# Performance work log

Measured on AMD Instinct MI355X. Metric: run time of the kernel, lower is better.

## Reference

```python
import jax, jax.numpy as jnp
import numpy as np

N, C, H, T, D, K = 4096, 512, 128, 64, 20, 10


def setup_inputs() -> dict:
    key = jax.random.key(0)
    ks = jax.random.split(key, 40)
    s = 0.05
    inp = {}
    inp["x"] = jax.random.normal(ks[0], (N, D * T), jnp.float32)
    inp["concept_matrix"] = (jax.random.uniform(ks[1], (N, C)) < 0.05).astype(jnp.float32)
    inp["market_value"] = jax.random.uniform(ks[2], (N,), jnp.float32) + 0.1
    # GRU params (torch layout: w_ih [3H,in], w_hh [3H,H], biases [3H]); 2 layers
    inp["gru_w_ih0"] = jax.random.normal(ks[3], (3 * H, D), jnp.float32) * s
    inp["gru_w_hh0"] = jax.random.normal(ks[4], (3 * H, H), jnp.float32) * s
    inp["gru_b_ih0"] = jax.random.normal(ks[5], (3 * H,), jnp.float32) * s
    inp["gru_b_hh0"] = jax.random.normal(ks[6], (3 * H,), jnp.float32) * s
    inp["gru_w_ih1"] = jax.random.normal(ks[7], (3 * H, H), jnp.float32) * s
    inp["gru_w_hh1"] = jax.random.normal(ks[8], (3 * H, H), jnp.float32) * s
    inp["gru_b_ih1"] = jax.random.normal(ks[9], (3 * H,), jnp.float32) * s
    inp["gru_b_hh1"] = jax.random.normal(ks[10], (3 * H,), jnp.float32) * s
    names = ["ps", "hs", "ps_fore", "hs_fore", "ps_back", "hs_back", "indi"]
    for i, n in enumerate(names):
        inp["w_" + n] = jax.random.normal(ks[11 + 2 * i], (H, H), jnp.float32) * s
        inp["b_" + n] = jax.random.normal(ks[12 + 2 * i], (H,), jnp.float32) * s
    inp["w_out"] = jax.random.normal(ks[30], (1, H), jnp.float32) * s
    inp["b_out"] = jax.random.normal(ks[31], (1,), jnp.float32) * s
    return inp


def _cos_sim(x, y):
    # x [n,d], y [m,d] -> [n,m]; NaN (0/0) replaced by 0 via safe denominator
    xy = x @ y.T
    nx = jnp.sqrt(jnp.sum(x * x, axis=1))[:, None]
    ny = jnp.sqrt(jnp.sum(y * y, axis=1))[:, None]
    return xy / jnp.maximum(nx @ ny.T, 1e-12)


def _gru_layer(seq, wih, whh, bih, bhh):
    # seq [T, n, in] -> outputs [T, n, H]
    n = seq.shape[1]
    h0 = jnp.zeros((n, whh.shape[1]), seq.dtype)

    def step(h, xt):
        gx = xt @ wih.T + bih
        gh = h @ whh.T + bhh
        gxr, gxz, gxn = jnp.split(gx, 3, axis=1)
        ghr, ghz, ghn = jnp.split(gh, 3, axis=1)
        r = jax.nn.sigmoid(gxr + ghr)
        z = jax.nn.sigmoid(gxz + ghz)
        ncand = jnp.tanh(gxn + r * ghn)
        hnew = (1.0 - z) * ncand + z * h
        return hnew, hnew

    _, out = jax.lax.scan(step, h0, seq)
    return out


def reference(x, concept_matrix, market_value,
              gru_w_ih0, gru_w_hh0, gru_b_ih0, gru_b_hh0,
              gru_w_ih1, gru_w_hh1, gru_b_ih1, gru_b_hh1,
              w_ps, b_ps, w_hs, b_hs, w_ps_fore, b_ps_fore, w_hs_fore, b_hs_fore,
              w_ps_back, b_ps_back, w_hs_back, b_hs_back, w_indi, b_indi,
              w_out, b_out):
    n = x.shape[0]
    # [n, D*T] -> [n, D, T] -> [n, T, D] -> [T, n, D]
    seq = jnp.swapaxes(x.reshape(n, D, -1).transpose(0, 2, 1), 0, 1)
    out0 = _gru_layer(seq, gru_w_ih0, gru_w_hh0, gru_b_ih0, gru_b_hh0)
    out1 = _gru_layer(out0, gru_w_ih1, gru_w_hh1, gru_b_ih1, gru_b_hh1)
    x_hidden = out1[-1]  # [n, H]

    # --- predefined-concept branch ---
    s2c = concept_matrix * market_value[:, None]
    s2c_den = jnp.sum(s2c, axis=0)[None, :] * concept_matrix + 1.0
    s2c = s2c / s2c_den
    hidden = s2c.T @ x_hidden  # [C, H]
    v1 = jnp.sum(hidden, axis=1) != 0  # valid concepts (replaces row filtering)
    s2c2 = jax.nn.softmax(x_hidden @ hidden.T, axis=0)  # [n, C], column-wise
    hidden2 = s2c2.T @ x_hidden  # [C, H]
    c2s = _cos_sim(x_hidden, hidden2)
    c2s = jax.nn.softmax(jnp.where(v1[None, :], c2s, -1e9), axis=1) * v1[None, :]
    p_shared = c2s @ hidden2
    p_shared = p_shared @ w_ps.T + b_ps
    p_back = p_shared @ w_ps_back.T + b_ps_back
    out_ps = jax.nn.leaky_relu(p_shared @ w_ps_fore.T + b_ps_fore)

    # --- hidden-concept branch ---
    h_shared = x_hidden - p_back
    hs2c = _cos_sim(h_shared, h_shared)  # [n, n]
    diag = jnp.diagonal(hs2c)
    hs2c = hs2c * (1.0 - jnp.eye(n, dtype=hs2c.dtype))
    _, idx = jax.lax.top_k(hs2c, K)  # [n, K]
    mask = jnp.zeros_like(hs2c).at[jnp.arange(n)[:, None], idx].set(1.0)
    hs2c = hs2c * mask
    hs2c = hs2c + jnp.diag((jnp.sum(hs2c, axis=0) != 0).astype(hs2c.dtype) * diag)
    hidden_h = (h_shared.T @ hs2c).T  # [n, H]
    v2 = jnp.sum(hidden_h, axis=1) != 0
    hc2s = _cos_sim(h_shared, hidden_h)
    hc2s = jax.nn.softmax(jnp.where(v2[None, :], hc2s, -1e9), axis=1) * v2[None, :]
    h_si = hc2s @ hidden_h
    h_si = h_si @ w_hs.T + b_hs
    h_back = h_si @ w_hs_back.T + b_hs_back
    out_hs = jax.nn.leaky_relu(h_si @ w_hs_fore.T + b_hs_fore)

    # --- individual branch + head ---
    indi = x_hidden - p_back - h_back
    out_indi = jax.nn.leaky_relu(indi @ w_indi.T + b_indi)
    all_info = out_ps + out_hs + out_indi
    return (all_info @ w_out.T + b_out).squeeze()
```

## Files before the change

### kernel.cpp

```cpp
#include <hip/hip_runtime.h>
#include <cstddef>

#define NR 4096
#define CDIM 512
#define HDIM 128
#define TSTEPS 64
#define DDIM 20
#define KTOP 10

typedef __attribute__((ext_vector_type(8))) short short8;
typedef __attribute__((ext_vector_type(4))) float f32x4;

__device__ __forceinline__ unsigned short f2bf(float f) {
    union { float f; unsigned u; } x; x.f = f;
    unsigned r = (x.u + 0x7fffu + ((x.u >> 16) & 1u)) >> 16;
    return (unsigned short)r;
}
__device__ __forceinline__ unsigned short f2bf_t(float f) {
    union { float f; unsigned u; } x; x.f = f;
    return (unsigned short)(x.u >> 16);
}
__device__ __forceinline__ float bf2f(unsigned short h) {
    union { unsigned u; float f; } x; x.u = ((unsigned)h) << 16;
    return x.f;
}
__device__ __forceinline__ float sigm(float v) {
    return __builtin_amdgcn_rcpf(1.f + __expf(-v));
}
__device__ __forceinline__ float tanh_f(float v) {
    return 1.f - 2.f * __builtin_amdgcn_rcpf(1.f + __expf(2.f * v));
}

#define MFMA16(a, b, c) __builtin_amdgcn_mfma_f32_16x16x32_bf16(a, b, c, 0, 0, 0)

struct MG {
    const float* A; const unsigned short* Bh; const unsigned short* Bl;
    const float* bias; float* C; const float* aux; float* sub;
    const unsigned short* Ah; const unsigned short* Al;
    const unsigned short* Bh2; const unsigned short* Bl2;
    const float* bias2; float* C2;
    const float* wout; const float* bout; float* hout;
    int N, K, kchunk, flags, flags2;
};

__global__ __launch_bounds__(256) void mfma_gemm(MG g)
{
    const int tid = threadIdx.x;
    const int w = tid >> 6, lane = tid & 63, quad = lane >> 4, lm = lane & 15;
    const int bm = (blockIdx.y << 6) + (w << 4);
    const int bn = blockIdx.x << 6;
    const int NC = g.K >> 5;
    int flags = g.flags;
    const unsigned short* Bh = g.Bh;
    const unsigned short* Bl = g.Bl;
    const float* bias = g.bias;
    float* C = g.C;
    int zk = blockIdx.z;
    if (g.flags & 32) {
        if (blockIdx.z) { Bh = g.Bh2; Bl = g.Bl2; bias = g.bias2; C = g.C2; flags = g.flags2; }
        zk = 0;
    }
    const int c0 = (zk * g.kchunk) >> 5;
    const int c1 = c0 + (g.kchunk >> 5);
    const float* arow = g.A + (size_t)(bm + lm) * g.K;
    const int packA = g.flags & 16;
    f32x4 acc[4];
    #pragma unroll
    for (int t = 0; t < 4; t++) acc[t] = (f32x4){0.f, 0.f, 0.f, 0.f};

    for (int c = c0; c < c1; c++) {
        short8 ah, al;
        if (packA) {
            size_t aidx = ((size_t)((bm >> 4) * NC + c) * 64 + lane) * 8;
            ah = *(const short8*)(g.Ah + aidx);
            al = *(const short8*)(g.Al + aidx);
        } else {
            const float* ap = arow + (c << 5) + (quad << 3);
            float4 a0 = *(const float4*)ap;
            float4 a1 = *(const float4*)(ap + 4);
            #pragma unroll
            for (int jj = 0; jj < 4; jj++) {
                float f = (&a0.x)[jj];
                unsigned short h = f2bf(f);
                ah[jj] = h; al[jj] = f2bf_t(f - bf2f(h));
                f = (&a1.x)[jj];
                h = f2bf(f);
                ah[4 + jj] = h; al[4 + jj] = f2bf_t(f - bf2f(h));
            }
        }
        #pragma unroll
        for (int t = 0; t < 4; t++) {
            size_t bidx = ((size_t)(((bn >> 4) + t) * NC + c) * 64 + lane) * 8;
            short8 bh = *(const short8*)(Bh + bidx);
            short8 bl = *(const short8*)(Bl + bidx);
            acc[t] = MFMA16(ah, bh, acc[t]);
            acc[t] = MFMA16(ah, bl, acc[t]);
            acc[t] = MFMA16(al, bh, acc[t]);
        }
    }
    float rsum[4] = {0.f, 0.f, 0.f, 0.f};
    #pragma unroll
    for (int t = 0; t < 4; t++) {
        #pragma unroll
        for (int rg = 0; rg < 4; rg++) {
            int row = bm + (quad << 2) + rg;
            int col = bn + (t << 4) + lm;
            float v = acc[t][rg];
            if (flags & 1) v += bias[col];
            if (flags & 2) v = v > 0.f ? v : 0.01f * v;
            if (flags & 64) rsum[rg] += v * g.wout[col];
            if (!(flags & 128)) {
                if (flags & 4) atomicAdd(&C[(size_t)row * g.N + col], v);
                else C[(size_t)row * g.N + col] = v;
            }
            if (flags & 8)
                g.sub[(size_t)row * g.N + col] = g.aux[(size_t)row * g.N + col] - v;
        }
    }
    if (flags & 64) {
        #pragma unroll
        for (int rg = 0; rg < 4; rg++) {
            #pragma unroll
            for (int d = 1; d < 16; d <<= 1) rsum[rg] += __shfl_xor(rsum[rg], d);
        }
        if (lm == 0) {
            #pragma unroll
            for (int rg = 0; rg < 4; rg++) {
                float s = rsum[rg];
                if ((flags & 256) && bn == 0) s += g.bout[0];
                atomicAdd(&g.hout[bm + (quad << 2) + rg], s);
            }
        }
    }
}

__global__ void pack_bt(const float* __restrict__ src, unsigned short* __restrict__ hi,
                        unsigned short* __restrict__ lo, int K, int total)
{
    int idx = blockIdx.x * 256 + threadIdx.x;
    if (idx >= total) return;
    int NC = K >> 5;
    int lane = idx & 63;
    int c = (idx >> 6) % NC;
    int t = idx / (NC * 64);
    int n = (t << 4) + (lane & 15);
    int kb = (c << 5) + ((lane >> 4) << 3);
    #pragma unroll
    for (int j = 0; j < 8; j++) {
        float f = src[(size_t)n * K + kb + j];
        unsigned short h = f2bf(f);
        hi[(size_t)idx * 8 + j] = h;
        lo[(size_t)idx * 8 + j] = f2bf_t(f - bf2f(h));
    }
}

__global__ void pack_both(const float* __restrict__ src,
                          unsigned short* __restrict__ bth, unsigned short* __restrict__ btl,
                          unsigned short* __restrict__ knh, unsigned short* __restrict__ knl,
                          int N, int total_kn)
{
    int idx = blockIdx.x * 256 + threadIdx.x;
    int lane = idx & 63;
    int totBT = (N >> 4) * 256;
    if (idx < totBT) {
        int c = (idx >> 6) & 3;
        int t = idx >> 8;
        int n = (t << 4) + (lane & 15);
        int kb = (c << 5) + ((lane >> 4) << 3);
        #pragma unroll
        for (int j = 0; j < 8; j++) {
            float f = src[(size_t)n * HDIM + kb + j];
            unsigned short h = f2bf(f);
            bth[(size_t)idx * 8 + j] = h;
            btl[(size_t)idx * 8 + j] = f2bf_t(f - bf2f(h));
        }
    }
    if (idx < total_kn) {
        int NC = N >> 5;
        int c = (idx >> 6) % NC;
        int t = idx / (NC * 64);
        int n = (t << 4) + (lane & 15);
        int kb = (c << 5) + ((lane >> 4) << 3);
        #pragma unroll
        for (int j = 0; j < 8; j++) {
            float f = src[(size_t)(kb + j) * HDIM + n];
            unsigned short h = f2bf(f);
            knh[(size_t)idx * 8 + j] = h;
            knl[(size_t)idx * 8 + j] = f2bf_t(f - bf2f(h));
        }
    }
}

struct W7 {
    const float* src[7];
    unsigned short* hi[7];
    unsigned short* lo[7];
};
__global__ void pack_w7(W7 p)
{
    int idx = blockIdx.x * 256 + threadIdx.x;
    if (idx >= 7 * 2048) return;
    int m = idx >> 11;
    int r = idx & 2047;
    int lane = r & 63;
    int c = (r >> 6) & 3;
    int t = r >> 8;
    int n = (t << 4) + (lane & 15);
    int kb = (c << 5) + ((lane >> 4) << 3);
    const float* src = p.src[m];
    unsigned short* hi = p.hi[m];
    unsigned short* lo = p.lo[m];
    #pragma unroll
    for (int j = 0; j < 8; j++) {
        float f = src[(size_t)n * HDIM + kb + j];
        unsigned short h = f2bf(f);
        hi[(size_t)r * 8 + j] = h;
        lo[(size_t)r * 8 + j] = f2bf_t(f - bf2f(h));
    }
}

__global__ __launch_bounds__(256) void scan_topk(const float* __restrict__ S,
        const float* __restrict__ hn, float* __restrict__ diagv,
        float* __restrict__ tvals, int* __restrict__ tidx)
{
    int row = blockIdx.x;
    const float* d = S + (size_t)row * NR;
    int tid = threadIdx.x;
    int wv = tid >> 6, lane = tid & 63;
    float hi_ = hn[row];
    float lv[16];
    #pragma unroll
    for (int i = 0; i < 16; i++) {
        int j = tid + (i << 8);
        float v = d[j] / fmaxf(hi_ * hn[j], 1e-12f);
        if (j == row) { diagv[row] = v; v = 0.f; }
        lv[i] = v;
    }
    __shared__ float sv[4];
    __shared__ int si[4];
    for (int k = 0; k < KTOP; k++) {
        float bv = -INFINITY; int bi = 0x7fffffff;
        #pragma unroll
        for (int i = 0; i < 16; i++) {
            int j = tid + (i << 8);
            if (lv[i] > bv || (lv[i] == bv && j < bi)) { bv = lv[i]; bi = j; }
        }
        #pragma unroll
        for (int m = 1; m < 64; m <<= 1) {
            float ov = __shfl_xor(bv, m); int oi = __shfl_xor(bi, m);
            if (ov > bv || (ov == bv && oi < bi)) { bv = ov; bi = oi; }
        }
        if (lane == 0) { sv[wv] = bv; si[wv] = bi; }
        __syncthreads();
        bv = sv[0]; bi = si[0];
        #pragma unroll
        for (int w = 1; w < 4; w++) {
            float ov = sv[w]; int oi = si[w];
            if (ov > bv || (ov == bv && oi < bi)) { bv = ov; bi = oi; }
        }
        if (tid == 0) { tvals[row * KTOP + k] = bv; tidx[row * KTOP + k] = bi; }
        if ((bi & 255) == tid) lv[bi >> 8] = -INFINITY;
        __syncthreads();
    }
}

__global__ __launch_bounds__(512) void hc2s_flash(
    const float* __restrict__ hsh, const float* __restrict__ hn,
    const float* __restrict__ hhn, const float* __restrict__ v2,
    const unsigned short* __restrict__ Bh, const unsigned short* __restrict__ Bl,
    const unsigned short* __restrict__ Vh, const unsigned short* __restrict__ Vl,
    float* __restrict__ pO, float* __restrict__ pM, float* __restrict__ pL)
{
    __shared__ __attribute__((aligned(16))) unsigned short Ph[8][16 * 72];
    __shared__ __attribute__((aligned(16))) unsigned short Plo[8][16 * 72];

    const int tid = threadIdx.x;
    const int wv = tid >> 6, lane = tid & 63, quad = lane >> 4, lm = lane & 15;
    const int rg2 = wv >> 1;
    const int cc = wv & 1;
    const int bm = (blockIdx.x << 6) + (rg2 << 4);
    const int rgg = (blockIdx.x << 2) + rg2;
    const int pidx = (blockIdx.y << 1) + cc;
    const int jt0 = (blockIdx.y << 4) + (cc << 3);

    short8 ahh[4], ahl[4];
    #pragma unroll
    for (int c = 0; c < 4; c++) {
        const float* ap = hsh + (size_t)(bm + lm) * HDIM + (c << 5) + (quad << 3);
        float4 a0 = *(const float4*)ap;
        float4 a1 = *(const float4*)(ap + 4);
        #pragma unroll
        for (int j = 0; j < 4; j++) {
            float f = (&a0.x)[j];
            unsigned short h = f2bf(f);
            ahh[c][j] = h; ahl[c][j] = f2bf_t(f - bf2f(h));
            f = (&a1.x)[j];
            h = f2bf(f);
            ahh[c][4 + j] = h; ahl[c][4 + j] = f2bf_t(f - bf2f(h));
        }
    }
    float hnr[4];
    #pragma unroll
    for (int rg = 0; rg < 4; rg++) hnr[rg] = hn[bm + (quad << 2) + rg];

    float m_old[4], l_old[4];
    #pragma unroll
    for (int rg = 0; rg < 4; rg++) { m_old[rg] = -INFINITY; l_old[rg] = 0.f; }
    f32x4 o[8];
    #pragma unroll
    for (int vt = 0; vt < 8; vt++) o[vt] = (f32x4){0.f, 0.f, 0.f, 0.f};

    const int pwr = lm * 72;
    for (int it = 0; it < 8; it++) {
        const int jt = jt0 + it;
        f32x4 s[4];
        #pragma unroll
        for (int tg = 0; tg < 4; tg++) {
            s[tg] = (f32x4){0.f, 0.f, 0.f, 0.f};
            #pragma unroll
            for (int c = 0; c < 4; c++) {
                size_t bidx = ((size_t)(((jt << 2) + tg) * 4 + c) * 64 + lane) * 8;
                short8 bh = *(const short8*)(Bh + bidx);
                short8 bl = *(const short8*)(Bl + bidx);
                s[tg] = MFMA16(ahh[c], bh, s[tg]);
                s[tg] = MFMA16(ahh[c], bl, s[tg]);
                s[tg] = MFMA16(ahl[c], bh, s[tg]);
            }
        }
        float sv[4][4];
        #pragma unroll
        for (int tg = 0; tg < 4; tg++) {
            int col = (jt << 6) + (tg << 4) + lm;
            float hc = hhn[col];
            float vm = v2[col];
            #pragma unroll
            for (int rg = 0; rg < 4; rg++) {
                float v = s[tg][rg] * __builtin_amdgcn_rcpf(fmaxf(hnr[rg] * hc, 1e-12f));
                sv[tg][rg] = (vm == 0.f) ? -1e9f : v;
            }
        }
        float m_new[4], alpha[4], tsum[4], pv[4][4];
        #pragma unroll
        for (int rg = 0; rg < 4; rg++) {
            float m = fmaxf(fmaxf(sv[0][rg], sv[1][rg]), fmaxf(sv[2][rg], sv[3][rg]));
            #pragma unroll
            for (int d = 1; d < 16; d <<= 1) m = fmaxf(m, __shfl_xor(m, d));
            m_new[rg] = fmaxf(m_old[rg], m);
            alpha[rg] = __expf(m_old[rg] - m_new[rg]);
        }
        #pragma unroll
        for (int rg = 0; rg < 4; rg++) {
            float p0_ = __expf(sv[0][rg] - m_new[rg]);
            float p1_ = __expf(sv[1][rg] - m_new[rg]);
            float p2_ = __expf(sv[2][rg] - m_new[rg]);
            float p3_ = __expf(sv[3][rg] - m_new[rg]);
            pv[0][rg] = p0_; pv[1][rg] = p1_; pv[2][rg] = p2_; pv[3][rg] = p3_;
            float ss = p0_ + p1_ + p2_ + p3_;
            #pragma unroll
            for (int d = 1; d < 16; d <<= 1) ss += __shfl_xor(ss, d);
            tsum[rg] = ss;
        }
        #pragma unroll
        for (int rg = 0; rg < 4; rg++) {
            l_old[rg] = l_old[rg] * alpha[rg] + tsum[rg];
            m_old[rg] = m_new[rg];
        }
        #pragma unroll
        for (int vt = 0; vt < 8; vt++) {
            #pragma unroll
            for (int rg = 0; rg < 4; rg++) o[vt][rg] *= alpha[rg];
        }
        #pragma unroll
        for (int tg = 0; tg < 4; tg++) {
            #pragma unroll
            for (int rg = 0; rg < 4; rg++) {
                int off = ((quad << 2) + rg) * 72 + (tg << 4) + lm;
                float p = pv[tg][rg];
                unsigned short h = f2bf(p);
                Ph[wv][off] = h;
                Plo[wv][off] = f2bf_t(p - bf2f(h));
            }
        }
        __asm__ volatile("s_waitcnt lgkmcnt(0)" ::: "memory");
        #pragma unroll
        for (int c2 = 0; c2 < 2; c2++) {
            int poff = pwr + (c2 << 5) + (quad << 3);
            short8 pah = *(const short8*)&Ph[wv][poff];
            short8 pal = *(const short8*)&Plo[wv][poff];
            int cg = (jt << 1) + c2;
            #pragma unroll
            for (int vt = 0; vt < 8; vt++) {
                size_t b0 = ((size_t)(vt * 128 + cg) * 64 + lane) * 8;
                short8 vh = *(const short8*)(Vh + b0);
                short8 vl = *(const short8*)(Vl + b0);
                o[vt] = MFMA16(pah, vh, o[vt]);
                o[vt] = MFMA16(pah, vl, o[vt]);
                o[vt] = MFMA16(pal, vh, o[vt]);
            }
        }
    }
    size_t pb = ((size_t)rgg * 8 + pidx) * 16;
    #pragma unroll
    for (int rg = 0; rg < 4; rg++) {
        int r = (quad << 2) + rg;
        #pragma unroll
        for (int vt = 0; vt < 8; vt++)
            pO[(pb + r) * 128 + (vt << 4) + lm] = o[vt][rg];
    }
    if (lm == 0) {
        #pragma unroll
        for (int rg = 0; rg < 4; rg++) {
            int r = (quad << 2) + rg;
            pM[pb + r] = m_old[rg];
            pL[pb + r] = l_old[rg];
        }
    }
}

__global__ __launch_bounds__(256) void hc2s_merge(const float* __restrict__ pO,
        const float* __restrict__ pM, const float* __restrict__ pL,
        float* __restrict__ O)
{
    int rgg = blockIdx.x;
    int tid = threadIdx.x;
    int r = tid >> 4;
    int c0 = (tid & 15) << 3;
    float m[8], e[8];
    float M = -INFINITY;
    #pragma unroll
    for (int i = 0; i < 8; i++) {
        m[i] = pM[((size_t)rgg * 8 + i) * 16 + r];
        M = fmaxf(M, m[i]);
    }
    float L = 0.f;
    #pragma unroll
    for (int i = 0; i < 8; i++) {
        e[i] = __expf(m[i] - M);
        L += pL[((size_t)rgg * 8 + i) * 16 + r] * e[i];
    }
    float invL = __builtin_amdgcn_rcpf(L);
    float a[8];
    #pragma unroll
    for (int k = 0; k < 8; k++) a[k] = 0.f;
    #pragma unroll
    for (int i = 0; i < 8; i++) {
        const float* src = pO + (((size_t)rgg * 8 + i) * 16 + r) * 128 + c0;
        float4 v0 = *(const float4*)src;
        float4 v1 = *(const float4*)(src + 4);
        a[0] += v0.x * e[i]; a[1] += v0.y * e[i]; a[2] += v0.z * e[i]; a[3] += v0.w * e[i];
        a[4] += v1.x * e[i]; a[5] += v1.y * e[i]; a[6] += v1.z * e[i]; a[7] += v1.w * e[i];
    }
    float* dst = O + ((size_t)rgg * 16 + r) * 128 + c0;
    #pragma unroll
    for (int k = 0; k < 8; k++) dst[k] = a[k] * invL;
}

__global__ void pack_wb(const float* __restrict__ W, unsigned short* __restrict__ Wp,
                        int K, int nch)
{
    int idx = blockIdx.x * 256 + threadIdx.x;
    if (idx >= 24 * nch * 64) return;
    int lane = idx & 63;
    int c = (idx >> 6) % nch;
    int t = idx / (nch * 64);
    int n = t * 16 + (lane & 15);
    int kb = c * 32 + (lane >> 4) * 8;
    #pragma unroll
    for (int j = 0; j < 8; j++) {
        int k = kb + j;
        float f = (k < K) ? W[(size_t)n * K + k] : 0.f;
        Wp[(size_t)idx * 8 + j] = f2bf(f);
    }
}

__global__ __launch_bounds__(512, 2) void gru_mfma(
    const float* __restrict__ xg,
    const unsigned short* __restrict__ wih0p,
    const unsigned short* __restrict__ whh0p,
    const unsigned short* __restrict__ wih1p,
    const unsigned short* __restrict__ whh1p,
    const float* __restrict__ bih0, const float* __restrict__ bhh0,
    const float* __restrict__ bih1, const float* __restrict__ bhh1,
    float* __restrict__ xh)
{
    __shared__ __attribute__((aligned(16))) unsigned short h0A[2][2][16 * 136];
    __shared__ __attribute__((aligned(16))) unsigned short h1A[2][2][16 * 136];
    __shared__ __attribute__((aligned(16))) unsigned short xA[2][2][16 * 40];

    const int tid = threadIdx.x;
    const int w2 = tid >> 6;
    const int lane = tid & 63;
    const int quad = lane >> 4;
    const int lm = lane & 15;
    const int n0 = blockIdx.x << 4;
    const int j = (w2 << 4) + lm;

    for (int i = tid; i < 2 * 2 * 16 * 136; i += 512) {
        ((unsigned short*)h0A)[i] = 0;
        ((unsigned short*)h1A)[i] = 0;
    }
    for (int i = tid; i < 2 * 2 * 16 * 40; i += 512) ((unsigned short*)xA)[i] = 0;

    float br0 = bih0[j] + bhh0[j];
    float bz0 = bih0[128 + j] + bhh0[128 + j];
    float bni0 = bih0[256 + j];
    float bnh0 = bhh0[256 + j];
    float br1 = bih1[j] + bhh1[j];
    float bz1 = bih1[128 + j] + bhh1[128 + j];
    float bni1 = bih1[256 + j];
    float bnh1 = bhh1[256 + j];

    short8 W0x[3], W0h[3][4], W1x[3][4], W1h[3][4];
    {
        const int lb = lane * 8;
        W0x[0] = *(const short8*)&wih0p[(size_t)(w2) * 512 + lb];
        W0x[1] = *(const short8*)&wih0p[(size_t)(8 + w2) * 512 + lb];
        W0x[2] = *(const short8*)&wih0p[(size_t)(16 + w2) * 512 + lb];
        #pragma unroll
        for (int c = 0; c < 4; c++) {
            W0h[0][c] = *(const short8*)&whh0p[(size_t)((w2) * 4 + c) * 512 + lb];
            W0h[1][c] = *(const short8*)&whh0p[(size_t)((8 + w2) * 4 + c) * 512 + lb];
            W0h[2][c] = *(const short8*)&whh0p[(size_t)((16 + w2) * 4 + c) * 512 + lb];
            W1x[0][c] = *(const short8*)&wih1p[(size_t)((w2) * 4 + c) * 512 + lb];
            W1x[1][c] = *(const short8*)&wih1p[(size_t)((8 + w2) * 4 + c) * 512 + lb];
            W1x[2][c] = *(const short8*)&wih1p[(size_t)((16 + w2) * 4 + c) * 512 + lb];
            W1h[0][c] = *(const short8*)&whh1p[(size_t)((w2) * 4 + c) * 512 + lb];
            W1h[1][c] = *(const short8*)&whh1p[(size_t)((8 + w2) * 4 + c) * 512 + lb];
            W1h[2][c] = *(const short8*)&whh1p[(size_t)((16 + w2) * 4 + c) * 512 + lb];
        }
    }

    const int aoff = lm * 136 + quad * 8;
    const int xoff = lm * 40 + quad * 8;
    const bool stager = tid < 16 * DDIM;
    const int sn = tid / DDIM, sd = tid % DDIM;
    const float* xrow = xg + (size_t)(n0 + sn) * (DDIM * TSTEPS) + sd * TSTEPS;
    const int soff = sn * 40 + sd;

    float h0reg[4] = {0.f, 0.f, 0.f, 0.f};
    float h1reg[4] = {0.f, 0.f, 0.f, 0.f};

    if (stager) {
        float v0 = xrow[0], v1 = xrow[1];
        unsigned short a = f2bf_t(v0);
        xA[0][0][soff] = a; xA[0][1][soff] = f2bf_t(v0 - bf2f(a));
        unsigned short b = f2bf_t(v1);
        xA[1][0][soff] = b; xA[1][1][soff] = f2bf_t(v1 - bf2f(b));
    }
    __syncthreads();

    {
        f32x4 accr = (f32x4){br0, br0, br0, br0};
        f32x4 accz = (f32x4){bz0, bz0, bz0, bz0};
        f32x4 accni = (f32x4){bni0, bni0, bni0, bni0};
        short8 axh = *(const short8*)&xA[0][0][xoff];
        short8 axl = *(const short8*)&xA[0][1][xoff];
        accr = MFMA16(axh, W0x[0], accr);
        accr = MFMA16(axl, W0x[0], accr);
        accz = MFMA16(axh, W0x[1], accz);
        accz = MFMA16(axl, W0x[1], accz);
        accni = MFMA16(axh, W0x[2], accni);
        accni = MFMA16(axl, W0x[2], accni);
        #pragma unroll
        for (int rg = 0; rg < 4; rg++) {
            float r = sigm(accr[rg]);
            float z = sigm(accz[rg]);
            float nc = tanh_f(accni[rg] + r * bnh0);
            float hnew = nc - z * nc;
            h0reg[rg] = hnew;
            int off = (quad * 4 + rg) * 136 + j;
            unsigned short hh_ = f2bf_t(hnew);
            h0A[0][0][off] = hh_;
            h0A[0][1][off] = f2bf_t(hnew - bf2f(hh_));
        }
    }
    __syncthreads();

#define GRU_IT(B, DO_L0, XT, LAST)                                                \
{                                                                                 \
    float xv = 0.f;                                                               \
    if ((XT) >= 0 && stager) xv = xrow[XT];          \
    f32x4 accr0 = (f32x4){br0, br0, br0, br0};                                    \
    f32x4 accz0 = (f32x4){bz0, bz0, bz0, bz0};                                    \
    f32x4 accni0 = (f32x4){bni0, bni0, bni0, bni0};                               \
    f32x4 accnh0 = (f32x4){bnh0, bnh0, bnh0, bnh0};                               \
    f32x4 accr1 = (f32x4){br1, br1, br1, br1};                                    \
    f32x4 accz1 = (f32x4){bz1, bz1, bz1, bz1};                                    \
    f32x4 accni1 = (f32x4){bni1, bni1, bni1, bni1};                               \
    f32x4 accnh1 = (f32x4){bnh1, bnh1, bnh1, bnh1};                               \
    if (DO_L0) {                                                                  \
        short8 axh = *(const short8*)&xA[(B) ^ 1][0][xoff];                       \
        short8 axl = *(const short8*)&xA[(B) ^ 1][1][xoff];                       \
        accr0 = MFMA16(axh, W0x[0], accr0);                                       \
        accr0 = MFMA16(axl, W0x[0], accr0);                                       \
        accz0 = MFMA16(axh, W0x[1], accz0);                                       \
        accz0 = MFMA16(axl, W0x[1], accz0);                                       \
        accni0 = MFMA16(axh, W0x[2], accni0);                                     \
        accni0 = MFMA16(axl, W0x[2], accni0);                                     \
    }                                                                             \
    _Pragma("unroll")                                                             \
    for (int c = 0; c < 4; c++) {                                                 \
        short8 a0h = *(const short8*)&h0A[B][0][aoff + c * 32];                   \
        short8 a0l = *(const short8*)&h0A[B][1][aoff + c * 32];                   \
        if (DO_L0) {                                                              \
            accr0 = MFMA16(a0h, W0h[0][c], accr0);                                \
            accr0 = MFMA16(a0l, W0h[0][c], accr0);                                \
            accz0 = MFMA16(a0h, W0h[1][c], accz0);                                \
            accz0 = MFMA16(a0l, W0h[1][c], accz0);                                \
            accnh0 = MFMA16(a0h, W0h[2][c], accnh0);                              \
            accnh0 = MFMA16(a0l, W0h[2][c], accnh0);                              \
        }                                                                         \
        accr1 = MFMA16(a0h, W1x[0][c], accr1);                                    \
        accr1 = MFMA16(a0l, W1x[0][c], accr1);                                    \
        accz1 = MFMA16(a0h, W1x[1][c], accz1);                                    \
        accz1 = MFMA16(a0l, W1x[1][c], accz1);                                    \
        accni1 = MFMA16(a0h, W1x[2][c], accni1);                                  \
        accni1 = MFMA16(a0l, W1x[2][c], accni1);                                  \
        short8 a1h = *(const short8*)&h1A[(B) ^ 1][0][aoff + c * 32];             \
        short8 a1l = *(const short8*)&h1A[(B) ^ 1][1][aoff + c * 32];             \
        accr1 = MFMA16(a1h, W1h[0][c], accr1);                                    \
        accr1 = MFMA16(a1l, W1h[0][c], accr1);                                    \
        accz1 = MFMA16(a1h, W1h[1][c], accz1);                                    \
        accz1 = MFMA16(a1l, W1h[1][c], accz1);                                    \
        accnh1 = MFMA16(a1h, W1h[2][c], accnh1);                                  \
        accnh1 = MFMA16(a1l, W1h[2][c], accnh1);                                  \
    }                                                                             \
    if (DO_L0) {                                                                  \
        _Pragma("unroll")                                                         \
        for (int rg = 0; rg < 4; rg++) {                                          \
            float r = sigm(accr0[rg]);                                            \
            float z = sigm(accz0[rg]);                                            \
            float nc = tanh_f(accni0[rg] + r * accnh0[rg]);                       \
            float hnew = nc + z * (h0reg[rg] - nc);                               \
            h0reg[rg] = hnew;                                                     \
            int off = (quad * 4 + rg) * 136 + j;                                  \
            unsigned short hh_ = f2bf_t(hnew);                                    \
            h0A[(B) ^ 1][0][off] = hh_;                                           \
            h0A[(B) ^ 1][1][off] = f2bf_t(hnew - bf2f(hh_));                      \
        }                                                                         \
    }                                                                             \
    _Pragma("unroll")                                                             \
    for (int rg = 0; rg < 4; rg++) {                                              \
        float r = sigm(accr1[rg]);                                                \
        float z = sigm(accz1[rg]);                                                \
        float nc = tanh_f(accni1[rg] + r * accnh1[rg]);                           \
        float hnew = nc + z * (h1reg[rg] - nc);                                   \
        h1reg[rg] = hnew;                                                         \
        if (LAST) {                                                               \
            xh[(size_t)(n0 + quad * 4 + rg) * HDIM + j] = hnew;                   \
        } else {                                                                  \
            int off = (quad * 4 + rg) * 136 + j;                                  \
            unsigned short hh_ = f2bf_t(hnew);                                    \
            h1A[B][0][off] = hh_;                                                 \
            h1A[B][1][off] = f2bf_t(hnew - bf2f(hh_));                            \
        }                                                                         \
    }                                                                             \
    if ((XT) >= 0 && stager) {                                                    \
        unsigned short hh_ = f2bf_t(xv);                                          \
        xA[B][0][soff] = hh_;                                                     \
        xA[B][1][soff] = f2bf_t(xv - bf2f(hh_));                                  \
    }                                                                             \
    if (!(LAST)) __syncthreads();                                                 \
}

    for (int i = 0; i < 62; i += 2) {
        GRU_IT(0, true, i + 2, false)
        GRU_IT(1, true, i + 3, false)
    }
    GRU_IT(0, true, -1, false)
    GRU_IT(1, false, -1, true)
#undef GRU_IT
}

__global__ __launch_bounds__(256) void den_atomic(const float* __restrict__ cm,
        const float* __restrict__ mv, float* __restrict__ den)
{
    int c = blockIdx.x * 64 + (threadIdx.x & 63);
    int rg = threadIdx.x >> 6;
    int nbase = blockIdx.y * 128;
    float acc = 0.f;
    for (int i = 0; i < 32; i++) {
        int n = nbase + rg + (i << 2);
        acc += cm[(size_t)n * CDIM + c] * mv[n];
    }
    __shared__ float red[4][64];
    red[rg][threadIdx.x & 63] = acc;
    __syncthreads();
    if (rg == 0)
        atomicAdd(&den[c], red[0][threadIdx.x] + red[1][threadIdx.x] +
                           red[2][threadIdx.x] + red[3][threadIdx.x]);
}

__global__ __launch_bounds__(256) void s2ct_trans(const float* __restrict__ cm,
        const float* __restrict__ mv, const float* __restrict__ den,
        float* __restrict__ s2cT)
{
    __shared__ float tile[64][65];
    __shared__ float mvs[64];
    const int tid = threadIdx.x;
    const int n0 = blockIdx.x << 6;
    const int c0 = blockIdx.y << 6;
    const int lc = tid & 63, lr = tid >> 6;
    if (tid < 64) mvs[tid] = mv[n0 + tid];
    #pragma unroll
    for (int i = 0; i < 16; i++) {
        int n = lr + (i << 2);
        tile[n][lc] = cm[(size_t)(n0 + n) * CDIM + c0 + lc];
    }
    __syncthreads();
    #pragma unroll
    for (int i = 0; i < 16; i++) {
        int c = lr + (i << 2);
        float m = tile[lc][c];
        float d = den[c0 + c];
        s2cT[(size_t)(c0 + c) * NR + n0 + lc] = (m * mvs[lc]) / (d * m + 1.f);
    }
}

__global__ void row_norm(const float* __restrict__ a, float* __restrict__ out)
{
    int r = blockIdx.x;
    float acc = 0.f;
    for (int h = threadIdx.x; h < HDIM; h += 64) {
        float v = a[(size_t)r * HDIM + h];
        acc += v * v;
    }
    for (int o = 32; o > 0; o >>= 1) acc += __shfl_down(acc, o);
    if (threadIdx.x == 0) out[r] = sqrtf(acc);
}

__global__ void row_nonzero(const float* __restrict__ a, float* __restrict__ out)
{
    int r = blockIdx.x;
    float acc = 0.f;
    for (int h = threadIdx.x; h < HDIM; h += 64) acc += a[(size_t)r * HDIM + h];
    for (int o = 32; o > 0; o >>= 1) acc += __shfl_down(acc, o);
    if (threadIdx.x == 0) out[r] = (acc != 0.f) ? 1.f : 0.f;
}

__global__ void row_norm_nz(const float* __restrict__ a, float* __restrict__ nrm,
                            float* __restrict__ nz)
{
    int r = blockIdx.x;
    float acc = 0.f, s = 0.f;
    for (int h = threadIdx.x; h < HDIM; h += 64) {
        float v = a[(size_t)r * HDIM + h];
        acc += v * v;
        s += v;
    }
    for (int o = 32; o > 0; o >>= 1) { acc += __shfl_down(acc, o); s += __shfl_down(s, o); }
    if (threadIdx.x == 0) { nrm[r] = sqrtf(acc); nz[r] = (s != 0.f) ? 1.f : 0.f; }
}

__global__ __launch_bounds__(256) void cos_softmax_row(float* __restrict__ data, int N,
        const float* __restrict__ rn, const float* __restrict__ cn,
        const float* __restrict__ vmask)
{
    int row = blockIdx.x;
    float* d = data + (size_t)row * N;
    int tid = threadIdx.x;
    int wv = tid >> 6, lane = tid & 63;
    __shared__ float red[8];
    float rnv = rn ? rn[row] : 0.f;
    float mx = -INFINITY;
    for (int j = tid; j < N; j += 256) {
        float v = d[j];
        if (cn) v = v * __builtin_amdgcn_rcpf(fmaxf(rnv * cn[j], 1e-12f));
        if (vmask && vmask[j] == 0.f) v = -1e9f;
        d[j] = v;
        mx = fmaxf(mx, v);
    }
    #pragma unroll
    for (int m = 1; m < 64; m <<= 1) mx = fmaxf(mx, __shfl_xor(mx, m));
    if (lane == 0) red[wv] = mx;
    __syncthreads();
    float M = fmaxf(fmaxf(red[0], red[1]), fmaxf(red[2], red[3]));
    float sum = 0.f;
    for (int j = tid; j < N; j += 256) {
        float e = __expf(d[j] - M);
        d[j] = e;
        sum += e;
    }
    #pragma unroll
    for (int m = 1; m < 64; m <<= 1) sum += __shfl_xor(sum, m);
    if (lane == 0) red[4 + wv] = sum;
    __syncthreads();
    float inv = __builtin_amdgcn_rcpf(red[4] + red[5] + red[6] + red[7]);
    for (int j = tid; j < N; j += 256) {
        float v = d[j] * inv;
        if (vmask) v *= vmask[j];
        d[j] = v;
    }
}

__global__ void hh_scatter(const float* __restrict__ vals, const int* __restrict__ idxs,
                           const float* __restrict__ hsh, float* __restrict__ hh,
                           float* __restrict__ colsum)
{
    int i = blockIdx.x;
    int t = threadIdx.x;
    float hv = hsh[(size_t)i * HDIM + t];
    #pragma unroll
    for (int k = 0; k < KTOP; k++) {
        int p = i * KTOP + k;
        int jj = idxs[p];
        float v = vals[p];
        atomicAdd(&hh[(size_t)jj * HDIM + t], v * hv);
    }
    if (t < KTOP) {
        int p = i * KTOP + t;
        atomicAdd(&colsum[idxs[p]], vals[p]);
    }
}

__global__ void hh_diag(const float* __restrict__ colsum, const float* __restrict__ diag,
                        const float* __restrict__ hsh, float* __restrict__ hh)
{
    int idx = blockIdx.x * 256 + threadIdx.x;
    int j = idx >> 7;
    if (colsum[j] != 0.f) hh[idx] += diag[j] * hsh[idx];
}

static inline void mg(hipStream_t s, const float* A, const unsigned short* Bh,
                      const unsigned short* Bl, const float* bias, float* C,
                      int M, int N, int K, int z, int flags,
                      const float* aux = nullptr, float* sub = nullptr,
                      const unsigned short* Ah = nullptr, const unsigned short* Al = nullptr,
                      const float* wout = nullptr, const float* bout = nullptr,
                      float* hout = nullptr)
{
    MG g{A, Bh, Bl, bias, C, aux, sub, Ah, Al,
         nullptr, nullptr, nullptr, nullptr, wout, bout, hout,
         N, K, K / z, flags | (z > 1 ? 4 : 0) | (Ah ? 16 : 0), 0};
    mfma_gemm<<<dim3(N / 64, M / 64, z), 256, 0, s>>>(g);
}
static inline void mg_dual(hipStream_t s, const float* A,
                           const unsigned short* Bh, const unsigned short* Bl,
                           const float* bias, float* C, int flags1,
                           const unsigned short* Bh2, const unsigned short* Bl2,
                           const float* bias2, float* C2, int flags2,
                           int M, int N, int K,
                           const float* aux, float* sub,
                           const float* wout, const float* bout, float* hout)
{
    MG g{A, Bh, Bl, bias, C, aux, sub, nullptr, nullptr,
         Bh2, Bl2, bias2, C2, wout, bout, hout,
         N, K, K, flags1 | 32, flags2};
    mfma_gemm<<<dim3(N / 64, M / 64, 2), 256, 0, s>>>(g);
}
static inline void pbt(hipStream_t s, const float* src, unsigned short* hi,
                       unsigned short* lo, int N, int K)
{
    int total = (N / 16) * (K / 32) * 64;
    pack_bt<<<(total + 255) / 256, 256, 0, s>>>(src, hi, lo, K, total);
}
static inline void pboth(hipStream_t s, const float* src,
                         unsigned short* bth, unsigned short* btl,
                         unsigned short* knh, unsigned short* knl, int N)
{
    int totBT = (N / 16) * 4 * 64;
    int totKN = 8 * (N / 32) * 64;
    int tot = totBT > totKN ? totBT : totKN;
    pack_both<<<(tot + 255) / 256, 256, 0, s>>>(src, bth, btl, knh, knl, N, totKN);
}

extern "C" void kernel_launch(void* const* d_in, const int* in_sizes, int n_in,
                              void* d_out, int out_size, void* d_ws, size_t ws_size,
                              hipStream_t stream)
{
    (void)in_sizes; (void)n_in; (void)out_size; (void)ws_size;
    const float* x    = (const float*)d_in[0];
    const float* cm   = (const float*)d_in[1];
    const float* mv   = (const float*)d_in[2];
    const float* wih0 = (const float*)d_in[3];
    const float* whh0 = (const float*)d_in[4];
    const float* bih0 = (const float*)d_in[5];
    const float* bhh0 = (const float*)d_in[6];
    const float* wih1 = (const float*)d_in[7];
    const float* whh1 = (const float*)d_in[8];
    const float* bih1 = (const float*)d_in[9];
    const float* bhh1 = (const float*)d_in[10];
    const float* w_ps = (const float*)d_in[11];
    const float* b_ps = (const float*)d_in[12];
    const float* w_hs = (const float*)d_in[13];
    const float* b_hs = (const float*)d_in[14];
    const float* w_ps_fore = (const float*)d_in[15];
    const float* b_ps_fore = (const float*)d_in[16];
    const float* w_hs_fore = (const float*)d_in[17];
    const float* b_hs_fore = (const float*)d_in[18];
    const float* w_ps_back = (const float*)d_in[19];
    const float* b_ps_back = (const float*)d_in[20];
    const float* w_hs_back = (const float*)d_in[21];
    const float* b_hs_back = (const float*)d_in[22];
    const float* w_indi = (const float*)d_in[23];
    const float* b_indi = (const float*)d_in[24];
    const float* w_out  = (const float*)d_in[25];
    const float* b_out  = (const float*)d_in[26];
    float* out = (float*)d_out;

    float* ws = (float*)d_ws;
    float* BIG = ws;
    float* zero0 = ws + 16777216;
    float* den      = zero0;
    float* hidden   = den + 512;
    float* hidden2  = hidden + 65536;
    float* colsum   = hidden2 + 65536;
    float* p0       = colsum + 4096;
    float* hidden_h = p0 + 524288;
    const size_t ZERO_FLOATS = 512 + 65536 + 65536 + 4096 + 524288 + 524288;
    float* h1 = hidden_h + 524288;
    float* v1 = h1 + 524288;
    float* xnorm = v1 + 512;
    float* h2n = xnorm + 4096;
    float* p_shared = h2n + 512;
    float* p_back = p_shared + 524288;
    float* h_shared = p_back + 524288;
    float* hn = h_shared + 524288;
    float* diagv = hn + 4096;
    float* tvals = diagv + 4096;
    int*   tidx = (int*)(tvals + 40960);
    float* v2 = (float*)(tidx + 40960);
    float* hhn = v2 + 4096;
    float* hsi0 = hhn + 4096;
    float* h_si = hsi0 + 524288;
    float* h_back = h_si + 524288;
    float* indi = h_back + 524288;
    float* extra = indi + 524288;

    unsigned short* wih0p = (unsigned short*)(BIG + 5242880);
    unsigned short* whh0p = wih0p + 12288;
    unsigned short* wih1p = whh0p + 49152;
    unsigned short* whh1p = wih1p + 49152;
    float* s2cT = BIG;
    float* L    = BIG + 2097152;
    float* c2s  = BIG + 4194304;
    unsigned short* PB = (unsigned short*)(BIG + 6291456);
    unsigned short* pbt_xh_hi = PB;
    unsigned short* pbt_xh_lo = pbt_xh_hi + 524288;
    unsigned short* pkn_xh_hi = pbt_xh_lo + 524288;
    unsigned short* pkn_xh_lo = pkn_xh_hi + 524288;
    unsigned short* pbt_h2_hi = pkn_xh_lo + 524288;
    unsigned short* pbt_h2_lo = pbt_h2_hi + 65536;
    unsigned short* pkn_h2_hi = pbt_h2_lo + 65536;
    unsigned short* pkn_h2_lo = pkn_h2_hi + 65536;
    unsigned short* wps_hi  = pkn_h2_lo + 65536;
    unsigned short* wps_lo  = wps_hi + 16384;
    unsigned short* wpsb_hi = wps_lo + 16384;
    unsigned short* wpsb_lo = wpsb_hi + 16384;
    unsigned short* wpsf_hi = wpsb_lo + 16384;
    unsigned short* wpsf_lo = wpsf_hi + 16384;
    unsigned short* pbt_hsh_hi = (unsigned short*)p0;
    unsigned short* pbt_hsh_lo = pbt_hsh_hi + 524288;
    unsigned short* pbt_hh_hi = (unsigned short*)indi;
    unsigned short* pbt_hh_lo = pbt_hh_hi + 524288;
    unsigned short* pkn_hh_hi = (unsigned short*)hsi0;
    unsigned short* pkn_hh_lo = pkn_hh_hi + 524288;
    float* part_O = BIG;
    float* part_m = BIG + 4194304;
    float* part_l = BIG + 4227072;
    unsigned short* EX = (unsigned short*)extra;
    unsigned short* whs_hi  = EX;            unsigned short* whs_lo  = EX + 16384;
    unsigned short* whsb_hi = EX + 32768;    unsigned short* whsb_lo = EX + 49152;
    unsigned short* whsf_hi = EX + 65536;    unsigned short* whsf_lo = EX + 81920;
    unsigned short* wind_hi = EX + 98304;    unsigned short* wind_lo = EX + 114688;

    hipMemsetAsync(zero0, 0, ZERO_FLOATS * sizeof(float), stream);
    hipMemsetAsync(out, 0, NR * sizeof(float), stream);

    pack_wb<<<6, 256, 0, stream>>>(wih0, wih0p, DDIM, 1);
    pack_wb<<<24, 256, 0, stream>>>(whh0, whh0p, HDIM, 4);
    pack_wb<<<24, 256, 0, stream>>>(wih1, wih1p, HDIM, 4);
    pack_wb<<<24, 256, 0, stream>>>(whh1, whh1p, HDIM, 4);
    {
        W7 w7;
        w7.src[0] = w_ps;      w7.hi[0] = wps_hi;  w7.lo[0] = wps_lo;
        w7.src[1] = w_ps_back; w7.hi[1] = wpsb_hi; w7.lo[1] = wpsb_lo;
        w7.src[2] = w_ps_fore; w7.hi[2] = wpsf_hi; w7.lo[2] = wpsf_lo;
        w7.src[3] = w_hs;      w7.hi[3] = whs_hi;  w7.lo[3] = whs_lo;
        w7.src[4] = w_hs_back; w7.hi[4] = whsb_hi; w7.lo[4] = whsb_lo;
        w7.src[5] = w_hs_fore; w7.hi[5] = whsf_hi; w7.lo[5] = whsf_lo;
        w7.src[6] = w_indi;    w7.hi[6] = wind_hi; w7.lo[6] = wind_lo;
        pack_w7<<<56, 256, 0, stream>>>(w7);
    }
    gru_mfma<<<NR / 16, 512, 0, stream>>>(x, wih0p, whh0p, wih1p, whh1p,
                                          bih0, bhh0, bih1, bhh1, h1);
    float* x_hidden = h1;

    den_atomic<<<dim3(CDIM / 64, 32), 256, 0, stream>>>(cm, mv, den);
    s2ct_trans<<<dim3(NR / 64, CDIM / 64), 256, 0, stream>>>(cm, mv, den, s2cT);
    pboth(stream, x_hidden, pbt_xh_hi, pbt_xh_lo, pkn_xh_hi, pkn_xh_lo, NR);
    mg(stream, s2cT, pkn_xh_hi, pkn_xh_lo, nullptr, hidden, CDIM, HDIM, NR, 16, 0);
    row_nonzero<<<CDIM, 64, 0, stream>>>(hidden, v1);
    mg(stream, hidden, pbt_xh_hi, pbt_xh_lo, nullptr, L, CDIM, NR, HDIM, 1, 0);
    cos_softmax_row<<<CDIM, 256, 0, stream>>>(L, NR, nullptr, nullptr, nullptr);
    mg(stream, L, pkn_xh_hi, pkn_xh_lo, nullptr, hidden2, CDIM, HDIM, NR, 16, 0);
    row_norm<<<NR, 64, 0, stream>>>(x_hidden, xnorm);
    row_norm<<<CDIM, 64, 0, stream>>>(hidden2, h2n);
    pboth(stream, hidden2, pbt_h2_hi, pbt_h2_lo, pkn_h2_hi, pkn_h2_lo, CDIM);
    mg(stream, x_hidden, pbt_h2_hi, pbt_h2_lo, nullptr, c2s, NR, CDIM, HDIM, 1, 0,
       nullptr, nullptr, pbt_xh_hi, pbt_xh_lo);
    cos_softmax_row<<<NR, 256, 0, stream>>>(c2s, CDIM, xnorm, h2n, v1);
    mg(stream, c2s, pkn_h2_hi, pkn_h2_lo, nullptr, p0, NR, HDIM, CDIM, 4, 0);
    mg(stream, p0, wps_hi, wps_lo, b_ps, p_shared, NR, HDIM, HDIM, 1, 1);
    mg_dual(stream, p_shared,
            wpsb_hi, wpsb_lo, b_ps_back, p_back, 1 | 8,
            wpsf_hi, wpsf_lo, b_ps_fore, nullptr, 1 | 2 | 64 | 128,
            NR, HDIM, HDIM, x_hidden, h_shared, w_out, b_out, out);

    row_norm<<<NR, 64, 0, stream>>>(h_shared, hn);
    pbt(stream, h_shared, pbt_hsh_hi, pbt_hsh_lo, NR, HDIM);
    mg(stream, h_shared, pbt_hsh_hi, pbt_hsh_lo, nullptr, BIG, NR, NR, HDIM, 1, 0,
       nullptr, nullptr, pbt_hsh_hi, pbt_hsh_lo);
    scan_topk<<<NR, 256, 0, stream>>>(BIG, hn, diagv, tvals, tidx);
    hh_scatter<<<NR, HDIM, 0, stream>>>(tvals, tidx, h_shared, hidden_h, colsum);
    hh_diag<<<2048, 256, 0, stream>>>(colsum, diagv, h_shared, hidden_h);
    row_norm_nz<<<NR, 64, 0, stream>>>(hidden_h, hhn, v2);
    pboth(stream, hidden_h, pbt_hh_hi, pbt_hh_lo, pkn_hh_hi, pkn_hh_lo, NR);
    hc2s_flash<<<dim3(NR / 64, 4), 512, 0, stream>>>(h_shared, hn, hhn, v2,
                                                     pbt_hh_hi, pbt_hh_lo,
                                                     pkn_hh_hi, pkn_hh_lo,
                                                     part_O, part_m, part_l);
    hc2s_merge<<<NR / 16, 256, 0, stream>>>(part_O, part_m, part_l, hsi0);
    mg(stream, hsi0, whs_hi, whs_lo, b_hs, h_si, NR, HDIM, HDIM, 1, 1);
    mg_dual(stream, h_si,
            whsb_hi, whsb_lo, b_hs_back, h_back, 1 | 8,
            whsf_hi, whsf_lo, b_hs_fore, nullptr, 1 | 2 | 64 | 128,
            NR, HDIM, HDIM, h_shared, indi, w_out, b_out, out);

    mg(stream, indi, wind_hi, wind_lo, b_indi, nullptr, NR, HDIM, HDIM, 1,
       1 | 2 | 64 | 128 | 256, nullptr, nullptr, nullptr, nullptr,
       w_out, b_out, out);
}
```

Baseline: 697.1 us.

## Merge weight-pack kernels, reorder GRU MFMAs, split-K small bias GEMMs

The four pack_wb launches and pack_w7 become a single pack_all kernel, which cuts launch overhead. In the GRU, MFMA issue order is interleaved so that independent accumulators sit between dependent ones, and the h1 LDS loads are hoisted earlier to hide MFMA dependency latency. The two 128x128 projection GEMMs now use split-K of 2 with atomic accumulation. To support that, bias is added only by the first K-split and p_shared/h_si move into the zeroed region. The atomics add contention and make the summation order nondeterministic.

```diff
diff --git a/kernel.cpp b/kernel.cpp
--- a/kernel.cpp
+++ b/kernel.cpp
@@ -106,7 +106,7 @@
             int row = bm + (quad << 2) + rg;
             int col = bn + (t << 4) + lm;
             float v = acc[t][rg];
-            if (flags & 1) v += bias[col];
+            if ((flags & 1) && (!(flags & 4) || zk == 0)) v += bias[col];
             if (flags & 2) v = v > 0.f ? v : 0.01f * v;
             if (flags & 64) rsum[rg] += v * g.wout[col];
             if (!(flags & 128)) {
@@ -191,31 +191,60 @@
     }
 }
 
-struct W7 {
-    const float* src[7];
-    unsigned short* hi[7];
-    unsigned short* lo[7];
+struct PAll {
+    const float* wb_src[4];
+    unsigned short* wb_dst[4];
+    const float* w7_src[7];
+    unsigned short* w7_hi[7];
+    unsigned short* w7_lo[7];
 };
-__global__ void pack_w7(W7 p)
+__global__ void pack_all(PAll p)
 {
     int idx = blockIdx.x * 256 + threadIdx.x;
-    if (idx >= 7 * 2048) return;
-    int m = idx >> 11;
-    int r = idx & 2047;
-    int lane = r & 63;
-    int c = (r >> 6) & 3;
-    int t = r >> 8;
-    int n = (t << 4) + (lane & 15);
-    int kb = (c << 5) + ((lane >> 4) << 3);
-    const float* src = p.src[m];
-    unsigned short* hi = p.hi[m];
-    unsigned short* lo = p.lo[m];
-    #pragma unroll
-    for (int j = 0; j < 8; j++) {
-        float f = src[(size_t)n * HDIM + kb + j];
-        unsigned short h = f2bf(f);
-        hi[(size_t)r * 8 + j] = h;
-        lo[(size_t)r * 8 + j] = f2bf_t(f - bf2f(h));
+    const int WB_END = 1536 + 3 * 6144;
+    if (idx < WB_END) {
+        int m, base, nch, K;
+        if (idx < 1536) { m = 0; base = 0; nch = 1; K = DDIM; }
+        else {
+            int q = (idx - 1536) / 6144;
+            m = 1 + q;
+            base = 1536 + q * 6144;
+            nch = 4; K = HDIM;
+        }
+        int r = idx - base;
+        int lane = r & 63;
+        int c = (r >> 6) % nch;
+        int t = r / (nch * 64);
+        int n = t * 16 + (lane & 15);
+        int kb = c * 32 + (lane >> 4) * 8;
+        const float* W = p.wb_src[m];
+        unsigned short* Wp = p.wb_dst[m];
+        #pragma unroll
+        for (int j = 0; j < 8; j++) {
+            int k = kb + j;
+            float f = (k < K) ? W[(size_t)n * K + k] : 0.f;
+            Wp[(size_t)r * 8 + j] = f2bf(f);
+        }
+    } else {
+        int q = idx - WB_END;
+        if (q >= 7 * 2048) return;
+        int m = q >> 11;
+        int r = q & 2047;
+        int lane = r & 63;
+        int c = (r >> 6) & 3;
+        int t = r >> 8;
+        int n = (t << 4) + (lane & 15);
+        int kb = (c << 5) + ((lane >> 4) << 3);
+        const float* src = p.w7_src[m];
+        unsigned short* hi = p.w7_hi[m];
+        unsigned short* lo = p.w7_lo[m];
+        #pragma unroll
+        for (int j = 0; j < 8; j++) {
+            float f = src[(size_t)n * HDIM + kb + j];
+            unsigned short h = f2bf(f);
+            hi[(size_t)r * 8 + j] = h;
+            lo[(size_t)r * 8 + j] = f2bf_t(f - bf2f(h));
+        }
     }
 }
 
@@ -455,24 +484,6 @@
     for (int k = 0; k < 8; k++) dst[k] = a[k] * invL;
 }
 
-__global__ void pack_wb(const float* __restrict__ W, unsigned short* __restrict__ Wp,
-                        int K, int nch)
-{
-    int idx = blockIdx.x * 256 + threadIdx.x;
-    if (idx >= 24 * nch * 64) return;
-    int lane = idx & 63;
-    int c = (idx >> 6) % nch;
-    int t = idx / (nch * 64);
-    int n = t * 16 + (lane & 15);
-    int kb = c * 32 + (lane >> 4) * 8;
-    #pragma unroll
-    for (int j = 0; j < 8; j++) {
-        int k = kb + j;
-        float f = (k < K) ? W[(size_t)n * K + k] : 0.f;
-        Wp[(size_t)idx * 8 + j] = f2bf(f);
-    }
-}
-
 __global__ __launch_bounds__(512, 2) void gru_mfma(
     const float* __restrict__ xg,
     const unsigned short* __restrict__ wih0p,
@@ -556,10 +567,10 @@
         short8 axh = *(const short8*)&xA[0][0][xoff];
         short8 axl = *(const short8*)&xA[0][1][xoff];
         accr = MFMA16(axh, W0x[0], accr);
+        accz = MFMA16(axh, W0x[1], accz);
+        accni = MFMA16(axh, W0x[2], accni);
         accr = MFMA16(axl, W0x[0], accr);
-        accz = MFMA16(axh, W0x[1], accz);
         accz = MFMA16(axl, W0x[1], accz);
-        accni = MFMA16(axh, W0x[2], accni);
         accni = MFMA16(axl, W0x[2], accni);
         #pragma unroll
         for (int rg = 0; rg < 4; rg++) {
@@ -592,37 +603,43 @@
         short8 axh = *(const short8*)&xA[(B) ^ 1][0][xoff];                       \
         short8 axl = *(const short8*)&xA[(B) ^ 1][1][xoff];                       \
         accr0 = MFMA16(axh, W0x[0], accr0);                                       \
+        accz0 = MFMA16(axh, W0x[1], accz0);                                       \
+        accni0 = MFMA16(axh, W0x[2], accni0);                                     \
         accr0 = MFMA16(axl, W0x[0], accr0);                                       \
-        accz0 = MFMA16(axh, W0x[1], accz0);                                       \
         accz0 = MFMA16(axl, W0x[1], accz0);                                       \
-        accni0 = MFMA16(axh, W0x[2], accni0);                                     \
         accni0 = MFMA16(axl, W0x[2], accni0);                                     \
     }                                                                             \
     _Pragma("unroll")                                                             \
     for (int c = 0; c < 4; c++) {                                                 \
         short8 a0h = *(const short8*)&h0A[B][0][aoff + c * 32];                   \
         short8 a0l = *(const short8*)&h0A[B][1][aoff + c * 32];                   \
+        short8 a1h = *(const short8*)&h1A[(B) ^ 1][0][aoff + c * 32];             \
+        short8 a1l = *(const short8*)&h1A[(B) ^ 1][1][aoff + c * 32];             \
+                \
         if (DO_L0) {                                                              \
             accr0 = MFMA16(a0h, W0h[0][c], accr0);                                \
+            accz0 = MFMA16(a0h, W0h[1][c], accz0);                                \
+            accnh0 = MFMA16(a0h, W0h[2][c], accnh0);                              \
+        }                                                                         \
+        accr1 = MFMA16(a0h, W1x[0][c], accr1);                                    \
+        accz1 = MFMA16(a0h, W1x[1][c], accz1);                                    \
+        accni1 = MFMA16(a0h, W1x[2][c], accni1);                                  \
+                                                                    \
+        if (DO_L0) {                                                              \
             accr0 = MFMA16(a0l, W0h[0][c], accr0);                                \
-            accz0 = MFMA16(a0h, W0h[1][c], accz0);                                \
             accz0 = MFMA16(a0l, W0h[1][c], accz0);                                \
-            accnh0 = MFMA16(a0h, W0h[2][c], accnh0);                              \
             accnh0 = MFMA16(a0l, W0h[2][c], accnh0);                              \
         }                                                                         \
-        accr1 = MFMA16(a0h, W1x[0][c], accr1);                                    \
         accr1 = MFMA16(a0l, W1x[0][c], accr1);                                    \
-        accz1 = MFMA16(a0h, W1x[1][c], accz1);                                    \
         accz1 = MFMA16(a0l, W1x[1][c], accz1);                                    \
-        accni1 = MFMA16(a0h, W1x[2][c], accni1);                                  \
         accni1 = MFMA16(a0l, W1x[2][c], accni1);                                  \
-        short8 a1h = *(const short8*)&h1A[(B) ^ 1][0][aoff + c * 32];             \
-        short8 a1l = *(const short8*)&h1A[(B) ^ 1][1][aoff + c * 32];             \
+                                                                    \
         accr1 = MFMA16(a1h, W1h[0][c], accr1);                                    \
+        accz1 = MFMA16(a1h, W1h[1][c], accz1);                                    \
+        accnh1 = MFMA16(a1h, W1h[2][c], accnh1);                                  \
+                                                                    \
         accr1 = MFMA16(a1l, W1h[0][c], accr1);                                    \
-        accz1 = MFMA16(a1h, W1h[1][c], accz1);                                    \
         accz1 = MFMA16(a1l, W1h[1][c], accz1);                                    \
-        accnh1 = MFMA16(a1h, W1h[2][c], accnh1);                                  \
         accnh1 = MFMA16(a1l, W1h[2][c], accnh1);                                  \
     }                                                                             \
     if (DO_L0) {                                                                  \
@@ -907,13 +924,14 @@
     float* colsum   = hidden2 + 65536;
     float* p0       = colsum + 4096;
     float* hidden_h = p0 + 524288;
-    const size_t ZERO_FLOATS = 512 + 65536 + 65536 + 4096 + 524288 + 524288;
-    float* h1 = hidden_h + 524288;
+    float* p_shared = hidden_h + 524288;
+    float* h_si     = p_shared + 524288;
+    const size_t ZERO_FLOATS = 512 + 65536 + 65536 + 4096 + 4 * 524288;
+    float* h1 = h_si + 524288;
     float* v1 = h1 + 524288;
     float* xnorm = v1 + 512;
     float* h2n = xnorm + 4096;
-    float* p_shared = h2n + 512;
-    float* p_back = p_shared + 524288;
+    float* p_back = h2n + 512;
     float* h_shared = p_back + 524288;
     float* hn = h_shared + 524288;
     float* diagv = hn + 4096;
@@ -922,8 +940,7 @@
     float* v2 = (float*)(tidx + 40960);
     float* hhn = v2 + 4096;
     float* hsi0 = hhn + 4096;
-    float* h_si = hsi0 + 524288;
-    float* h_back = h_si + 524288;
+    float* h_back = hsi0 + 524288;
     float* indi = h_back + 524288;
     float* extra = indi + 524288;
 
@@ -967,20 +984,20 @@
     hipMemsetAsync(zero0, 0, ZERO_FLOATS * sizeof(float), stream);
     hipMemsetAsync(out, 0, NR * sizeof(float), stream);
 
-    pack_wb<<<6, 256, 0, stream>>>(wih0, wih0p, DDIM, 1);
-    pack_wb<<<24, 256, 0, stream>>>(whh0, whh0p, HDIM, 4);
-    pack_wb<<<24, 256, 0, stream>>>(wih1, wih1p, HDIM, 4);
-    pack_wb<<<24, 256, 0, stream>>>(whh1, whh1p, HDIM, 4);
     {
-        W7 w7;
-        w7.src[0] = w_ps;      w7.hi[0] = wps_hi;  w7.lo[0] = wps_lo;
-        w7.src[1] = w_ps_back; w7.hi[1] = wpsb_hi; w7.lo[1] = wpsb_lo;
-        w7.src[2] = w_ps_fore; w7.hi[2] = wpsf_hi; w7.lo[2] = wpsf_lo;
-        w7.src[3] = w_hs;      w7.hi[3] = whs_hi;  w7.lo[3] = whs_lo;
-        w7.src[4] = w_hs_back; w7.hi[4] = whsb_hi; w7.lo[4] = whsb_lo;
-        w7.src[5] = w_hs_fore; w7.hi[5] = whsf_hi; w7.lo[5] = whsf_lo;
-        w7.src[6] = w_indi;    w7.hi[6] = wind_hi; w7.lo[6] = wind_lo;
-        pack_w7<<<56, 256, 0, stream>>>(w7);
+        PAll pa;
+        pa.wb_src[0] = wih0; pa.wb_dst[0] = wih0p;
+        pa.wb_src[1] = whh0; pa.wb_dst[1] = whh0p;
+        pa.wb_src[2] = wih1; pa.wb_dst[2] = wih1p;
+        pa.wb_src[3] = whh1; pa.wb_dst[3] = whh1p;
+        pa.w7_src[0] = w_ps;      pa.w7_hi[0] = wps_hi;  pa.w7_lo[0] = wps_lo;
+        pa.w7_src[1] = w_ps_back; pa.w7_hi[1] = wpsb_hi; pa.w7_lo[1] = wpsb_lo;
+        pa.w7_src[2] = w_ps_fore; pa.w7_hi[2] = wpsf_hi; pa.w7_lo[2] = wpsf_lo;
+        pa.w7_src[3] = w_hs;      pa.w7_hi[3] = whs_hi;  pa.w7_lo[3] = whs_lo;
+        pa.w7_src[4] = w_hs_back; pa.w7_hi[4] = whsb_hi; pa.w7_lo[4] = whsb_lo;
+        pa.w7_src[5] = w_hs_fore; pa.w7_hi[5] = whsf_hi; pa.w7_lo[5] = whsf_lo;
+        pa.w7_src[6] = w_indi;    pa.w7_hi[6] = wind_hi; pa.w7_lo[6] = wind_lo;
+        pack_all<<<134, 256, 0, stream>>>(pa);
     }
     gru_mfma<<<NR / 16, 512, 0, stream>>>(x, wih0p, whh0p, wih1p, whh1p,
                                           bih0, bhh0, bih1, bhh1, h1);
@@ -1001,7 +1018,7 @@
        nullptr, nullptr, pbt_xh_hi, pbt_xh_lo);
     cos_softmax_row<<<NR, 256, 0, stream>>>(c2s, CDIM, xnorm, h2n, v1);
     mg(stream, c2s, pkn_h2_hi, pkn_h2_lo, nullptr, p0, NR, HDIM, CDIM, 4, 0);
-    mg(stream, p0, wps_hi, wps_lo, b_ps, p_shared, NR, HDIM, HDIM, 1, 1);
+    mg(stream, p0, wps_hi, wps_lo, b_ps, p_shared, NR, HDIM, HDIM, 2, 1);
     mg_dual(stream, p_shared,
             wpsb_hi, wpsb_lo, b_ps_back, p_back, 1 | 8,
             wpsf_hi, wpsf_lo, b_ps_fore, nullptr, 1 | 2 | 64 | 128,
@@ -1021,7 +1038,7 @@
                                                      pkn_hh_hi, pkn_hh_lo,
                                                      part_O, part_m, part_l);
     hc2s_merge<<<NR / 16, 256, 0, stream>>>(part_O, part_m, part_l, hsi0);
-    mg(stream, hsi0, whs_hi, whs_lo, b_hs, h_si, NR, HDIM, HDIM, 1, 1);
+    mg(stream, hsi0, whs_hi, whs_lo, b_hs, h_si, NR, HDIM, HDIM, 2, 1);
     mg_dual(stream, h_si,
             whsb_hi, whsb_lo, b_hs_back, h_back, 1 | 8,
             whsf_hi, whsf_lo, b_hs_fore, nullptr, 1 | 2 | 64 | 128,
```

New measurement: 671.4 us (median of 2 runs). 3.7% less time.
